# Kernel optimization log

Measured on AMD Instinct MI355X. Metric: run time of the kernel, lower is better.

The kernel has to match this reference:

```python
import jax, jax.numpy as jnp
import numpy as np

SCALE = 1.0
DENSE = 4
ITERS = 5


def setup_inputs() -> dict:
    key = jax.random.key(0)
    k1, k2, k3 = jax.random.split(key, 3)
    data = jax.random.normal(k1, (8, 32, 512, 512), dtype=jnp.float32)
    # nonnegative marginal attention maps (strictly positive to keep sums safe)
    attx = jax.random.uniform(k2, (8, 512, 1), dtype=jnp.float32, minval=0.01, maxval=1.0)
    atty = jax.random.uniform(k3, (8, 512, 1), dtype=jnp.float32, minval=0.01, maxval=1.0)
    return {"data": data, "attx": attx, "atty": atty}


def _axis_coords(att, out_size):
    """Iterative clipped inverse-CDF sampling coords (AttSamplerGrid math).

    att: (N, S) nonnegative marginal attention. Returns coords in [-1, 1], (N, out_size).
    """
    N, S = att.shape
    att = att / jnp.sum(att, axis=1, keepdims=True) * out_size  # sum == out_size
    thr = DENSE * out_size / S  # each input cell maps to at most `dense` output pixels
    for _ in range(ITERS):
        att = jnp.minimum(att, thr)
        # redistribute clipped mass uniformly so the sum returns to out_size
        att = att + (out_size - jnp.sum(att, axis=1, keepdims=True)) / S
    csum = jnp.cumsum(att, axis=1)                      # (N, S) monotone CDF * out_size
    step = csum[:, -1:] / out_size                      # (N, 1), ~1.0
    tgt = step * jnp.arange(1, out_size + 1, dtype=att.dtype)[None, :]  # (N, out)
    # first index j with csum[j] >= target  (inverse CDF)
    j = jax.vmap(lambda c, t: jnp.searchsorted(c, t, side='left'))(csum, tgt)
    j = jnp.clip(j, 0, S - 1)
    right = jnp.take_along_axis(csum, j, axis=1)
    left = jnp.where(j > 0, jnp.take_along_axis(csum, jnp.maximum(j - 1, 0), axis=1), 0.0)
    frac = jnp.clip((tgt - left) / jnp.maximum(right - left, 1e-8), 0.0, 1.0)
    return (j.astype(att.dtype) + frac) / S * 2.0 - 1.0


def _lerp_axis(x, coord, axis):
    """1-D linear interpolation of x along `axis` at normalized coords in [-1,1].

    x: (N, C, H, W); coord: (N, L). align_corners=True mapping, coords stay in-range
    so zero-padding never triggers (bilinear grid_sample is separable for this grid).
    """
    size = x.shape[axis]
    p = (coord + 1.0) * 0.5 * (size - 1)
    p0f = jnp.floor(p)
    w = p - p0f                                         # (N, L)
    i0 = jnp.clip(p0f.astype(jnp.int32), 0, size - 1)
    i1 = jnp.clip(i0 + 1, 0, size - 1)
    shp = [coord.shape[0], 1, 1, 1]
    shp[axis] = coord.shape[1]
    i0 = i0.reshape(shp)
    i1 = i1.reshape(shp)
    w = w.reshape(shp)
    x0 = jnp.take_along_axis(x, i0, axis=axis)
    x1 = jnp.take_along_axis(x, i1, axis=axis)
    return x0 * (1.0 - w) + x1 * w


def reference(data, attx, atty):
    N, C, H, W = data.shape
    out_h = int(round(H * SCALE))
    out_w = int(round(W * SCALE))
    gx = _axis_coords(attx[..., 0], out_w)   # (N, out_w) x-coords (width)
    gy = _axis_coords(atty[..., 0], out_h)   # (N, out_h) y-coords (height)
    cols = _lerp_axis(data, gx, axis=3)      # (N, C, H, out_w)
    out = _lerp_axis(cols, gy, axis=2)       # (N, C, out_h, out_w)
    return out
```

## Files before the change

kernel.cpp:

```cpp
#include <hip/hip_runtime.h>

#define S    512
#define OUT  512
#define NB   8
#define CB   32
#define TRW  16
#define NBLK (NB * CB * 8)

__global__ __launch_bounds__(64) void coords_kernel(
    const float* __restrict__ attx, const float* __restrict__ atty,
    int2* __restrict__ coords)
{
  __shared__ double sc[S];
  const int lane = threadIdx.x;
  const int n    = blockIdx.x & 7;
  const int axis = blockIdx.x >> 3;
  const float* att = (axis == 0 ? attx : atty) + n * S;

  double a[8];
#pragma unroll
  for (int k = 0; k < 8; ++k) a[k] = (double)att[lane * 8 + k];

  double tot = 0.0;
#pragma unroll
  for (int k = 0; k < 8; ++k) tot += a[k];
#pragma unroll
  for (int off = 32; off > 0; off >>= 1) tot += __shfl_xor(tot, off);

#pragma unroll
  for (int k = 0; k < 8; ++k) a[k] = a[k] / tot * (double)OUT;
  const double thr = (double)(4 * OUT) / (double)S;

  for (int it = 0; it < 5; ++it) {
    double s = 0.0;
#pragma unroll
    for (int k = 0; k < 8; ++k) { a[k] = a[k] < thr ? a[k] : thr; s += a[k]; }
#pragma unroll
    for (int off = 32; off > 0; off >>= 1) s += __shfl_xor(s, off);
    const double corr = ((double)OUT - s) / (double)S;
#pragma unroll
    for (int k = 0; k < 8; ++k) a[k] += corr;
  }

  double p[8]; double run = 0.0;
#pragma unroll
  for (int k = 0; k < 8; ++k) { run += a[k]; p[k] = run; }
  double v = run;
#pragma unroll
  for (int off = 1; off < 64; off <<= 1) {
    double t = __shfl_up(v, off);
    if (lane >= off) v += t;
  }
  const double excl = v - run;
#pragma unroll
  for (int k = 0; k < 8; ++k) sc[lane * 8 + k] = excl + p[k];
  __syncthreads();

  const double step = sc[S - 1] / (double)OUT;

#pragma unroll
  for (int k = 0; k < 8; ++k) {
    const int ox = lane * 8 + k;
    const double tgt = step * (double)(ox + 1);

    int lo = 0, hi = S;
    while (lo < hi) {
      int mid = (lo + hi) >> 1;
      if (sc[mid] < tgt) lo = mid + 1; else hi = mid;
    }
    int j = lo < S - 1 ? lo : S - 1;

    double right = sc[j];
    double left  = (j > 0) ? sc[j - 1] : 0.0;
    double denom = right - left;
    if (denom < 1e-8) denom = 1e-8;
    double frac = (tgt - left) / denom;
    frac = frac < 0.0 ? 0.0 : (frac > 1.0 ? 1.0 : frac);

    double pp  = ((double)j + frac) / (double)S * (double)(S - 1);
    double p0f = floor(pp);
    double w   = pp - p0f;
    int i0 = (int)p0f;
    i0 = i0 < 0 ? 0 : (i0 > S - 1 ? S - 1 : i0);

    coords[(axis * NB + n) * S + ox] = make_int2(i0, __float_as_int((float)w));
  }
}

__global__ __launch_bounds__(256) void sample_kernel(
    const float* __restrict__ data, const int2* __restrict__ coords,
    float* __restrict__ out)
{
  __shared__ float bufA_[4][S + 1];
  __shared__ float bufB_[4][S + 1];

  int b = (int)blockIdx.x;
  b = (b & 7) * (NBLK / 8) + (b >> 3);
  const int plane = b >> 3;
  const int bip   = b & 7;
  const int n     = plane >> 5;

  const int tid  = threadIdx.x;
  const int wv   = tid >> 6;
  const int lane = tid & 63;
  const int oy0  = bip * 64 + wv * TRW;

  const float* __restrict__ pl = data + (size_t)plane * (S * S);
  float* __restrict__       po = out  + (size_t)plane * (S * S);

  int   ix[8];
  float wx[8];
#pragma unroll
  for (int k = 0; k < 8; ++k) {
    const int2 cx = coords[n * S + lane + 64 * k];
    ix[k] = cx.x;
    wx[k] = __int_as_float(cx.y);
  }

  float* bufA = bufA_[wv];
  float* bufB = bufB_[wv];
  const int2* __restrict__ cyp = coords + (NB + n) * S + oy0;

  float CxA[8], CxB[8];
  int curA = -1000;

  for (int r = 0; r < TRW; ++r) {
    const int2 cy = cyp[r];
    const int   a  = cy.x;
    const float wy = __int_as_float(cy.y);

    if (a != curA) {
      const int rowB = (a + 1 < S) ? a + 1 : S - 1;
      if (a == curA + 1) {
#pragma unroll
        for (int k = 0; k < 8; ++k) CxA[k] = CxB[k];
        const float4* RB = (const float4*)(pl + (size_t)rowB * S);
        const float4 p0 = RB[lane];
        const float4 p1 = RB[lane + 64];
        ((float4*)bufB)[lane]      = p0;
        ((float4*)bufB)[lane + 64] = p1;
        if (lane == 63) bufB[S] = p1.w;
#pragma unroll
        for (int k = 0; k < 8; ++k) {
          const float x0 = bufB[ix[k]];
          const float x1 = bufB[ix[k] + 1];
          CxB[k] = x0 + wx[k] * (x1 - x0);
        }
      } else {
        const float4* RA = (const float4*)(pl + (size_t)a    * S);
        const float4* RB = (const float4*)(pl + (size_t)rowB * S);
        const float4 q0 = RA[lane];
        const float4 q1 = RA[lane + 64];
        const float4 p0 = RB[lane];
        const float4 p1 = RB[lane + 64];
        ((float4*)bufA)[lane]      = q0;
        ((float4*)bufA)[lane + 64] = q1;
        ((float4*)bufB)[lane]      = p0;
        ((float4*)bufB)[lane + 64] = p1;
        if (lane == 63) { bufA[S] = q1.w; bufB[S] = p1.w; }
#pragma unroll
        for (int k = 0; k < 8; ++k) {
          const float x0 = bufA[ix[k]];
          const float x1 = bufA[ix[k] + 1];
          CxA[k] = x0 + wx[k] * (x1 - x0);
        }
#pragma unroll
        for (int k = 0; k < 8; ++k) {
          const float x0 = bufB[ix[k]];
          const float x1 = bufB[ix[k] + 1];
          CxB[k] = x0 + wx[k] * (x1 - x0);
        }
      }
      curA = a;
    }

    float* orow = po + (size_t)(oy0 + r) * OUT;
#pragma unroll
    for (int k = 0; k < 8; ++k)
      __builtin_nontemporal_store(CxA[k] + wy * (CxB[k] - CxA[k]),
                                  orow + lane + 64 * k);
  }
}

extern "C" void kernel_launch(void* const* d_in, const int* in_sizes, int n_in,
                              void* d_out, int out_size, void* d_ws, size_t ws_size,
                              hipStream_t stream) {
  const float* data = (const float*)d_in[0];
  const float* attx = (const float*)d_in[1];
  const float* atty = (const float*)d_in[2];
  float* out = (float*)d_out;

  int2* coords = (int2*)d_ws;

  coords_kernel<<<16, 64, 0, stream>>>(attx, atty, coords);

  sample_kernel<<<NBLK, 256, 0, stream>>>(data, coords, out);
}
```

Baseline: 104.7 us.

## Software-pipeline row loads two iterations ahead in sample kernel

Prefetches the global rows needed for output rows r+2 into registers while row r is processed, using a two-slot ring of float4 registers and a per-slot transition type. This is meant to hide global load latency behind the LDS writes and horizontal interpolation of the current row. In exchange, register pressure rises (up to 16 extra float4 values plus a fully unrolled loop), which may lower occupancy.

```diff
diff --git a/kernel.cpp b/kernel.cpp
--- a/kernel.cpp
+++ b/kernel.cpp
@@ -122,56 +122,105 @@
   const int2* __restrict__ cyp = coords + (NB + n) * S + oy0;
 
   float CxA[8], CxB[8];
-  int curA = -1000;
-
+  float4 qA0[2], qA1[2], qB0[2], qB1[2];
+  int   ttype[2];
+  float wys[2];
+  int prevA;
+
+  {
+    const int2 c = cyp[0];
+    const int a = c.x;
+    wys[0] = __int_as_float(c.y);
+    const int rb = (a + 1 < S) ? a + 1 : S - 1;
+    const float4* RA = (const float4*)(pl + (size_t)a  * S);
+    const float4* RB = (const float4*)(pl + (size_t)rb * S);
+    qA0[0] = RA[lane]; qA1[0] = RA[lane + 64];
+    qB0[0] = RB[lane]; qB1[0] = RB[lane + 64];
+    ttype[0] = 2;
+    prevA = a;
+  }
+  {
+    const int2 c = cyp[1];
+    const int a = c.x;
+    wys[1] = __int_as_float(c.y);
+    if (a == prevA) {
+      ttype[1] = 0;
+    } else {
+      const int rb = (a + 1 < S) ? a + 1 : S - 1;
+      const float4* RB = (const float4*)(pl + (size_t)rb * S);
+      qB0[1] = RB[lane]; qB1[1] = RB[lane + 64];
+      if (a == prevA + 1) {
+        ttype[1] = 1;
+      } else {
+        const float4* RA = (const float4*)(pl + (size_t)a * S);
+        qA0[1] = RA[lane]; qA1[1] = RA[lane + 64];
+        ttype[1] = 2;
+      }
+      prevA = a;
+    }
+  }
+
+#pragma unroll
   for (int r = 0; r < TRW; ++r) {
-    const int2 cy = cyp[r];
-    const int   a  = cy.x;
-    const float wy = __int_as_float(cy.y);
-
-    if (a != curA) {
-      const int rowB = (a + 1 < S) ? a + 1 : S - 1;
-      if (a == curA + 1) {
-#pragma unroll
-        for (int k = 0; k < 8; ++k) CxA[k] = CxB[k];
-        const float4* RB = (const float4*)(pl + (size_t)rowB * S);
-        const float4 p0 = RB[lane];
-        const float4 p1 = RB[lane + 64];
-        ((float4*)bufB)[lane]      = p0;
-        ((float4*)bufB)[lane + 64] = p1;
-        if (lane == 63) bufB[S] = p1.w;
-#pragma unroll
-        for (int k = 0; k < 8; ++k) {
-          const float x0 = bufB[ix[k]];
-          const float x1 = bufB[ix[k] + 1];
-          CxB[k] = x0 + wx[k] * (x1 - x0);
+    const int s = r & 1;
+    const int t = ttype[s];
+    const float wy = wys[s];
+
+    if (t == 2) {
+      ((float4*)bufA)[lane]      = qA0[s];
+      ((float4*)bufA)[lane + 64] = qA1[s];
+      ((float4*)bufB)[lane]      = qB0[s];
+      ((float4*)bufB)[lane + 64] = qB1[s];
+      if (lane == 63) { bufA[S] = qA1[s].w; bufB[S] = qB1[s].w; }
+    } else if (t == 1) {
+      ((float4*)bufB)[lane]      = qB0[s];
+      ((float4*)bufB)[lane + 64] = qB1[s];
+      if (lane == 63) bufB[S] = qB1[s].w;
+    }
+
+    if (r + 2 < TRW) {
+      const int2 c = cyp[r + 2];
+      const int a = c.x;
+      wys[s] = __int_as_float(c.y);
+      if (a == prevA) {
+        ttype[s] = 0;
+      } else {
+        const int rb = (a + 1 < S) ? a + 1 : S - 1;
+        const float4* RB = (const float4*)(pl + (size_t)rb * S);
+        qB0[s] = RB[lane]; qB1[s] = RB[lane + 64];
+        if (a == prevA + 1) {
+          ttype[s] = 1;
+        } else {
+          const float4* RA = (const float4*)(pl + (size_t)a * S);
+          qA0[s] = RA[lane]; qA1[s] = RA[lane + 64];
+          ttype[s] = 2;
         }
-      } else {
-        const float4* RA = (const float4*)(pl + (size_t)a    * S);
-        const float4* RB = (const float4*)(pl + (size_t)rowB * S);
-        const float4 q0 = RA[lane];
-        const float4 q1 = RA[lane + 64];
-        const float4 p0 = RB[lane];
-        const float4 p1 = RB[lane + 64];
-        ((float4*)bufA)[lane]      = q0;
-        ((float4*)bufA)[lane + 64] = q1;
-        ((float4*)bufB)[lane]      = p0;
-        ((float4*)bufB)[lane + 64] = p1;
-        if (lane == 63) { bufA[S] = q1.w; bufB[S] = p1.w; }
-#pragma unroll
-        for (int k = 0; k < 8; ++k) {
-          const float x0 = bufA[ix[k]];
-          const float x1 = bufA[ix[k] + 1];
-          CxA[k] = x0 + wx[k] * (x1 - x0);
-        }
-#pragma unroll
-        for (int k = 0; k < 8; ++k) {
-          const float x0 = bufB[ix[k]];
-          const float x1 = bufB[ix[k] + 1];
-          CxB[k] = x0 + wx[k] * (x1 - x0);
-        }
-      }
-      curA = a;
+        prevA = a;
+      }
+    }
+
+    if (t == 2) {
+#pragma unroll
+      for (int k = 0; k < 8; ++k) {
+        const float x0 = bufA[ix[k]];
+        const float x1 = bufA[ix[k] + 1];
+        CxA[k] = x0 + wx[k] * (x1 - x0);
+      }
+#pragma unroll
+      for (int k = 0; k < 8; ++k) {
+        const float x0 = bufB[ix[k]];
+        const float x1 = bufB[ix[k] + 1];
+        CxB[k] = x0 + wx[k] * (x1 - x0);
+      }
+    } else if (t == 1) {
+#pragma unroll
+      for (int k = 0; k < 8; ++k) CxA[k] = CxB[k];
+#pragma unroll
+      for (int k = 0; k < 8; ++k) {
+        const float x0 = bufB[ix[k]];
+        const float x1 = bufB[ix[k] + 1];
+        CxB[k] = x0 + wx[k] * (x1 - x0);
+      }
     }
 
     float* orow = po + (size_t)(oy0 + r) * OUT;
```

Result: slower. 193.0 us (+84.3%).
